# Kernel optimization log

Measured on AMD Instinct MI355X. Metric: run time of the kernel, lower is better.

The kernel has to match this reference:

```python
import jax, jax.numpy as jnp
import numpy as np


def setup_inputs() -> dict:
    key = jax.random.key(0)
    kq, kk, kv = jax.random.split(key, 3)
    B, H, S, d = 2, 16, 2048, 64
    return {
        "query": jax.random.normal(kq, (B, H, S, d), dtype=jnp.float32),
        "keys": jax.random.normal(kk, (B, H, S, d), dtype=jnp.float32),
        "vals": jax.random.normal(kv, (B, H, S, d), dtype=jnp.float32),
    }


def reference(query, keys, vals):
    # SE (RBF-like) kernel attention, include_magnitude=True, p=2, dropout=0 (eval).
    d = query.shape[-1]
    scale = 2.0 * (d ** 0.5)
    q2 = jnp.sum(query * query, axis=-1)  # [B,H,Sq] = ||q||^2
    k2 = jnp.sum(keys * keys, axis=-1)    # [B,H,Sk] = ||k||^2
    qk = jnp.einsum("bhqd,bhkd->bhqk", query, keys)  # [B,H,Sq,Sk]
    # ||q-k||^2 = ||q||^2 - 2 q.k + ||k||^2 ; clamp for numerical safety
    sq_dist = jnp.maximum(q2[..., :, None] - 2.0 * qk + k2[..., None, :], 0.0)
    dist = jnp.sqrt(sq_dist)  # L2 norm (NOT squared), as in torch.norm(diff, p=2)
    # preattn = -||q-k|| / (2 sqrt(d)) + (||q||^2 + ||k||^2) / (2 sqrt(d))
    preattn = (-dist + q2[..., :, None] + k2[..., None, :]) / scale
    attn = jax.nn.softmax(preattn, axis=-1)  # [B,H,Sq,Sk]
    return jnp.einsum("bhqk,bhkd->bhqd", attn, vals)
```

## Files before the change

kernel.cpp:

```cpp
#include <hip/hip_runtime.h>
#include <hip/hip_bf16.h>
#include <math.h>


typedef __attribute__((ext_vector_type(8))) short bf16x8;
typedef __attribute__((ext_vector_type(4))) float f32x4;
typedef __attribute__((ext_vector_type(16))) float f32x16;
typedef __attribute__((ext_vector_type(4))) unsigned int uint32x4;
typedef __attribute__((ext_vector_type(2))) unsigned int uint32x2;

#define SEQ    2048
#define DIM    64
#define NHEAD  32
#define QBLK   128
#define KVB    64
#define NKT    (SEQ / KVB)
#define TILE_B 8192
#define C2     0.0901684403f

__device__ __forceinline__ float fast_exp2(float x) { return __builtin_amdgcn_exp2f(x); }
__device__ __forceinline__ float fast_sqrt(float x) { return __builtin_amdgcn_sqrtf(x); }

__device__ __forceinline__ unsigned int f2bf(float f) {
    __hip_bfloat16 h = __float2bfloat16(f);
    unsigned short u;
    __builtin_memcpy(&u, &h, 2);
    return (unsigned int)u;
}

__device__ __forceinline__ bf16x8 pack4(unsigned a, unsigned b, unsigned c, unsigned d) {
    uint32x4 t; t[0] = a; t[1] = b; t[2] = c; t[3] = d;
    bf16x8 r;
    __builtin_memcpy(&r, &t, 16);
    return r;
}

__global__ __launch_bounds__(256, 4)
void prep_kv(const float* __restrict__ Kg, const float* __restrict__ Vg,
             char* __restrict__ Kp, char* __restrict__ Vp,
             float* __restrict__ k2g) {
    const int tid  = threadIdx.x;
    const int kt   = blockIdx.x;
    const int head = blockIdx.y;
    const size_t hb = (size_t)head * (SEQ * DIM);
    char* kdst = Kp + (size_t)(head * NKT + kt) * TILE_B;
    char* vdst = Vp + (size_t)(head * NKT + kt) * TILE_B;

    {
        const int row = tid >> 2;
        const int sc4 = tid & 3;
        const float* kp = Kg + hb + (size_t)(kt * KVB + row) * DIM + sc4 * 16;
        f32x4 a = *(const f32x4*)kp;
        f32x4 b = *(const f32x4*)(kp + 4);
        f32x4 c = *(const f32x4*)(kp + 8);
        f32x4 d = *(const f32x4*)(kp + 12);
        float part = 0.f;
#pragma unroll
        for (int j = 0; j < 4; ++j)
            part += a[j]*a[j] + b[j]*b[j] + c[j]*c[j] + d[j]*d[j];
        part += __shfl_xor(part, 1);
        part += __shfl_xor(part, 2);
        if (sc4 == 0) k2g[head * SEQ + kt * KVB + row] = part;

        bf16x8 p0, p1;
#pragma unroll
        for (int j = 0; j < 4; ++j) {
            p0[j]     = (short)f2bf(a[j]);
            p0[4 + j] = (short)f2bf(b[j]);
            p1[j]     = (short)f2bf(c[j]);
            p1[4 + j] = (short)f2bf(d[j]);
        }
        const int t = row >> 5;
        char* base = kdst + (t * 4 + sc4) * 1024 + (row & 31) * 16;
        *(bf16x8*)base         = p0;
        *(bf16x8*)(base + 512) = p1;
    }
    {
        const int kp_ = tid & 31;
        const int dg  = tid >> 5;
        const float* vp = Vg + hb + (size_t)(kt * KVB + 2 * kp_) * DIM + dg * 8;
        f32x4 a0 = *(const f32x4*)vp;
        f32x4 a1 = *(const f32x4*)(vp + 4);
        f32x4 b0 = *(const f32x4*)(vp + DIM);
        f32x4 b1 = *(const f32x4*)(vp + DIM + 4);
        const int ks   = kp_ >> 3;
        const int lh   = (kp_ >> 2) & 1;
        const int j    = kp_ & 3;
#pragma unroll
        for (int e = 0; e < 8; ++e) {
            const float lo = (e < 4) ? a0[e] : a1[e - 4];
            const float hi = (e < 4) ? b0[e] : b1[e - 4];
            const unsigned pk = f2bf(lo) | (f2bf(hi) << 16);
            const int d    = dg * 8 + e;
            const int half = d >> 5;
            const int l    = (d & 31) + 32 * lh;
            *(unsigned*)(vdst + (ks * 2 + half) * 1024 + l * 16 + j * 4) = pk;
        }
    }
}

__global__ __launch_bounds__(256, 2)
void se_attn_main(const float* __restrict__ Qg, const char* __restrict__ Kp,
                  const char* __restrict__ Vp, const float* __restrict__ k2g,
                  float* __restrict__ Og) {
    __shared__ float linv_sh[4][32];

    const int tid = threadIdx.x;
    const int w   = tid >> 6;
    const int l   = tid & 63;
    const int ql  = l & 31;
    const int hi  = l >> 5;

    const int bid  = blockIdx.x;
    const int wg   = (bid & 7) * 64 + (bid >> 3);
    const int head = wg >> 4;
    const int qb   = wg & 15;

    const size_t hb = (size_t)head * (SEQ * DIM);
    const int qbase = qb * QBLK + w * 32;

    const char*  Kph = Kp + (size_t)head * NKT * TILE_B;
    const char*  Vph = Vp + (size_t)head * NKT * TILE_B;
    const float* k2h = k2g + head * SEQ;

    bf16x8 qf[4];
    float q2 = 0.f;
#pragma unroll
    for (int s = 0; s < 4; ++s) {
        const float* qp = Qg + hb + (size_t)(qbase + ql) * DIM + s * 16 + hi * 8;
        f32x4 a = *(const f32x4*)qp;
        f32x4 b = *(const f32x4*)(qp + 4);
#pragma unroll
        for (int j = 0; j < 4; ++j) {
            q2 += a[j] * a[j] + b[j] * b[j];
            qf[s][j]     = (short)f2bf(a[j]);
            qf[s][4 + j] = (short)f2bf(b[j]);
        }
    }
    q2 += __shfl_xor(q2, 32);

    f32x16 o0, o1;
#pragma unroll
    for (int i = 0; i < 16; ++i) { o0[i] = 0.f; o1[i] = 0.f; }
    float lsA = 0.f, lsB = 0.f;

    const int loff = l * 16;

    for (int kt = 0; kt < NKT; ++kt) {
        const char* Kt = Kph + (size_t)kt * TILE_B;
        const char* Vt = Vph + (size_t)kt * TILE_B;

        f32x4 k2q[2][4];
#pragma unroll
        for (int t = 0; t < 2; ++t)
#pragma unroll
            for (int rq = 0; rq < 4; ++rq)
                k2q[t][rq] = *(const f32x4*)(k2h + kt * 64 + t * 32 + rq * 8 + 4 * hi);

        f32x16 st0, st1;
#pragma unroll
        for (int i = 0; i < 16; ++i) { st0[i] = 0.f; st1[i] = 0.f; }
        __builtin_amdgcn_s_setprio(1);
#pragma unroll
        for (int s = 0; s < 4; ++s) {
            bf16x8 kf0 = *(const bf16x8*)(Kt + (0 * 4 + s) * 1024 + loff);
            st0 = __builtin_amdgcn_mfma_f32_32x32x16_bf16(kf0, qf[s], st0, 0, 0, 0);
            bf16x8 kf1 = *(const bf16x8*)(Kt + (1 * 4 + s) * 1024 + loff);
            st1 = __builtin_amdgcn_mfma_f32_32x32x16_bf16(kf1, qf[s], st1, 0, 0, 0);
        }
        __builtin_amdgcn_s_setprio(0);

        bf16x8 vf0[4], vf1[4];
#pragma unroll
        for (int ks = 0; ks < 4; ++ks) {
            vf0[ks] = *(const bf16x8*)(Vt + (ks * 2 + 0) * 1024 + loff);
            vf1[ks] = *(const bf16x8*)(Vt + (ks * 2 + 1) * 1024 + loff);
        }

        unsigned cpk[2][4][2];
#pragma unroll
        for (int t = 0; t < 2; ++t) {
#pragma unroll
            for (int rq = 0; rq < 4; ++rq) {
                float pv[4];
#pragma unroll
                for (int r = 0; r < 4; ++r) {
                    const float dot = (t == 0) ? st0[rq * 4 + r] : st1[rq * 4 + r];
                    const float kk  = k2q[t][rq][r];
                    const float sq  = fmaxf(fmaf(-2.f, dot, q2 + kk), 0.f);
                    const float p   = fast_exp2(fmaf(-C2, fast_sqrt(sq), kk * C2));
                    if (r & 1) lsB += p; else lsA += p;
                    pv[r] = p;
                }
                cpk[t][rq][0] = f2bf(pv[0]) | (f2bf(pv[1]) << 16);
                cpk[t][rq][1] = f2bf(pv[2]) | (f2bf(pv[3]) << 16);
            }
        }

        bf16x8 pa[4];
#pragma unroll
        for (int t = 0; t < 2; ++t) {
#pragma unroll
            for (int e = 0; e < 2; ++e) {
                unsigned lo_[2][2], hi_[2][2];
#pragma unroll
                for (int po = 0; po < 2; ++po) {
#pragma unroll
                    for (int i = 0; i < 2; ++i) {
                        uint32x2 r2 = __builtin_amdgcn_permlane32_swap(
                            cpk[t][2 * e + po][i], cpk[t][2 * e + po][i], false, false);
                        lo_[po][i] = r2[0];
                        hi_[po][i] = r2[1];
                    }
                }
                const int ks = t * 2 + e;
                const unsigned u0 = hi ? lo_[1][0] : lo_[0][0];
                const unsigned u1 = hi ? lo_[1][1] : lo_[0][1];
                const unsigned u2 = hi ? hi_[1][0] : hi_[0][0];
                const unsigned u3 = hi ? hi_[1][1] : hi_[0][1];
                pa[ks] = pack4(u0, u1, u2, u3);
            }
        }

        __builtin_amdgcn_s_setprio(1);
#pragma unroll
        for (int ks = 0; ks < 4; ++ks) {
            o0 = __builtin_amdgcn_mfma_f32_32x32x16_bf16(pa[ks], vf0[ks], o0, 0, 0, 0);
            o1 = __builtin_amdgcn_mfma_f32_32x32x16_bf16(pa[ks], vf1[ks], o1, 0, 0, 0);
        }
        __builtin_amdgcn_s_setprio(0);
    }

    float ls = lsA + lsB;
    ls += __shfl_xor(ls, 32);
    const float inv = 1.f / ls;
    if (hi == 0) linv_sh[w][ql] = inv;
    f32x4 iq[4];
#pragma unroll
    for (int rq = 0; rq < 4; ++rq)
        iq[rq] = *(const f32x4*)(&linv_sh[w][rq * 8 + 4 * hi]);

#pragma unroll
    for (int reg = 0; reg < 16; ++reg) {
        const int qloc = (reg & 3) + 8 * (reg >> 2) + 4 * hi;
        float* orow = Og + hb + (size_t)(qbase + qloc) * DIM;
        const float s = iq[reg >> 2][reg & 3];
        orow[ql]      = o0[reg] * s;
        orow[32 + ql] = o1[reg] * s;
    }
}

__global__ __launch_bounds__(256, 4)
void se_attn_mfma(const float* __restrict__ Qg, const float* __restrict__ Kg,
                  const float* __restrict__ Vg, float* __restrict__ Og) {
    __shared__ char  Kl[KVB * 128];
    __shared__ char  Vt[DIM * 128];
    __shared__ char  Pl[4][16 * 128];
    __shared__ float k2s[KVB];

    const int tid = threadIdx.x;
    const int w   = tid >> 6;
    const int l   = tid & 63;
    const int lq  = l & 15;
    const int g   = l >> 4;
    const size_t hb = (size_t)blockIdx.y * (SEQ * DIM);
    const int q = blockIdx.x * 64 + w * 16 + lq;
    char* Pw = Pl[w];
    const int swq = (lq & 7) << 4;

    bf16x8 qf[2];
    float q2 = 0.f;
#pragma unroll
    for (int h = 0; h < 2; ++h) {
        const float* qp = Qg + hb + (size_t)q * DIM + h * 32 + g * 8;
        f32x4 a = *(const f32x4*)qp;
        f32x4 b = *(const f32x4*)(qp + 4);
#pragma unroll
        for (int j = 0; j < 4; ++j) {
            q2 += a[j] * a[j] + b[j] * b[j];
            qf[h][j]     = (short)f2bf(a[j]);
            qf[h][4 + j] = (short)f2bf(b[j]);
        }
    }
    q2 += __shfl_xor(q2, 16);
    q2 += __shfl_xor(q2, 32);

    f32x4 ofr[4];
#pragma unroll
    for (int i = 0; i < 4; ++i) ofr[i] = (f32x4){0.f, 0.f, 0.f, 0.f};
    float m = -INFINITY, lsum = 0.f;

    const int srow = tid >> 2;
    const int sc4  = tid & 3;
    const int vpr  = tid & 31;
    const int vd0  = (tid >> 5) * 8;

    for (int kt = 0; kt < NKT; ++kt) {
        __syncthreads();
        {
            const float* kp = Kg + hb + (size_t)(kt * KVB + srow) * DIM + sc4 * 16;
            f32x4 a = *(const f32x4*)kp;
            f32x4 b = *(const f32x4*)(kp + 4);
            f32x4 c = *(const f32x4*)(kp + 8);
            f32x4 d = *(const f32x4*)(kp + 12);
            float part = 0.f;
#pragma unroll
            for (int j = 0; j < 4; ++j)
                part += a[j]*a[j] + b[j]*b[j] + c[j]*c[j] + d[j]*d[j];
            part += __shfl_xor(part, 1);
            part += __shfl_xor(part, 2);
            if (sc4 == 0) k2s[srow] = part;
            bf16x8 p0, p1;
#pragma unroll
            for (int j = 0; j < 4; ++j) {
                p0[j]     = (short)f2bf(a[j]);
                p0[4 + j] = (short)f2bf(b[j]);
                p1[j]     = (short)f2bf(c[j]);
                p1[4 + j] = (short)f2bf(d[j]);
            }
            const int sw = (srow & 7) << 4;
            const int wa = srow * 128 + sc4 * 32;
            *(bf16x8*)(Kl + (wa ^ sw))        = p0;
            *(bf16x8*)(Kl + ((wa + 16) ^ sw)) = p1;
        }
        {
            const float* vp = Vg + hb + (size_t)(kt * KVB + 2 * vpr) * DIM + vd0;
            f32x4 a0 = *(const f32x4*)vp;
            f32x4 a1 = *(const f32x4*)(vp + 4);
            f32x4 b0 = *(const f32x4*)(vp + DIM);
            f32x4 b1 = *(const f32x4*)(vp + DIM + 4);
#pragma unroll
            for (int j = 0; j < 8; ++j) {
                const float lo = (j < 4) ? a0[j] : a1[j - 4];
                const float hi2 = (j < 4) ? b0[j] : b1[j - 4];
                const unsigned int pk = f2bf(lo) | (f2bf(hi2) << 16);
                const int d = vd0 + j;
                const int wa = d * 128 + vpr * 4;
                *(unsigned int*)(Vt + (wa ^ ((d & 7) << 4))) = pk;
            }
        }
        __syncthreads();

        f32x4 st[4];
#pragma unroll
        for (int f = 0; f < 4; ++f) st[f] = (f32x4){0.f, 0.f, 0.f, 0.f};
#pragma unroll
        for (int f = 0; f < 4; ++f) {
#pragma unroll
            for (int h = 0; h < 2; ++h) {
                const int ra = (f * 16 + lq) * 128 + h * 64 + g * 16;
                bf16x8 kf = *(const bf16x8*)(Kl + (ra ^ swq));
                st[f] = __builtin_amdgcn_mfma_f32_16x16x32_bf16(kf, qf[h], st[f], 0, 0, 0);
            }
        }

        float sc[4][4];
        float tmax = -INFINITY;
#pragma unroll
        for (int f = 0; f < 4; ++f) {
            const f32x4 k2v = *(const f32x4*)(k2s + f * 16 + g * 4);
#pragma unroll
            for (int r = 0; r < 4; ++r) {
                const float kk = k2v[r];
                const float sq = fmaxf(fmaf(-2.f, st[f][r], q2 + kk), 0.f);
                const float s  = (kk - sqrtf(sq)) * 0.0625f;
                sc[f][r] = s;
                tmax = fmaxf(tmax, s);
            }
        }
        tmax = fmaxf(tmax, __shfl_xor(tmax, 16));
        tmax = fmaxf(tmax, __shfl_xor(tmax, 32));
        const float nm    = fmaxf(m, tmax);
        const float scale = __expf(m - nm);
        m = nm;
        lsum *= scale;
#pragma unroll
        for (int i = 0; i < 4; ++i) {
            ofr[i][0] *= scale; ofr[i][1] *= scale;
            ofr[i][2] *= scale; ofr[i][3] *= scale;
        }
#pragma unroll
        for (int f = 0; f < 4; ++f) {
#pragma unroll
            for (int e = 0; e < 2; ++e) {
                const float p0 = __expf(sc[f][2 * e]     - m);
                const float p1 = __expf(sc[f][2 * e + 1] - m);
                lsum += p0 + p1;
                const unsigned int pk = f2bf(p0) | (f2bf(p1) << 16);
                const int pr = 8 * f + 2 * g + e;
                const int wa = lq * 128 + pr * 4;
                *(unsigned int*)(Pw + (wa ^ swq)) = pk;
            }
        }

        bf16x8 pf[2];
#pragma unroll
        for (int h = 0; h < 2; ++h) {
            const int ra = lq * 128 + h * 64 + g * 16;
            pf[h] = *(const bf16x8*)(Pw + (ra ^ swq));
        }
#pragma unroll
        for (int db = 0; db < 4; ++db) {
#pragma unroll
            for (int h = 0; h < 2; ++h) {
                const int ra = (db * 16 + lq) * 128 + h * 64 + g * 16;
                bf16x8 vf = *(const bf16x8*)(Vt + (ra ^ swq));
                ofr[db] = __builtin_amdgcn_mfma_f32_16x16x32_bf16(vf, pf[h], ofr[db], 0, 0, 0);
            }
        }
    }

    lsum += __shfl_xor(lsum, 16);
    lsum += __shfl_xor(lsum, 32);
    const float inv = 1.f / lsum;
    float* op = Og + hb + (size_t)q * DIM;
#pragma unroll
    for (int db = 0; db < 4; ++db) {
#pragma unroll
        for (int r = 0; r < 4; ++r) {
            op[db * 16 + g * 4 + r] = ofr[db][r] * inv;
        }
    }
}

extern "C" void kernel_launch(void* const* d_in, const int* in_sizes, int n_in,
                              void* d_out, int out_size, void* d_ws, size_t ws_size,
                              hipStream_t stream) {
    const float* Q = (const float*)d_in[0];
    const float* K = (const float*)d_in[1];
    const float* V = (const float*)d_in[2];
    float* O = (float*)d_out;

    const size_t KP_B = (size_t)NHEAD * NKT * TILE_B;
    const size_t K2_B = (size_t)NHEAD * SEQ * 4;
    const size_t need = 2 * KP_B + K2_B;

    if (ws_size >= need) {
        char*  Kp = (char*)d_ws;
        char*  Vp = Kp + KP_B;
        float* k2 = (float*)(Kp + 2 * KP_B);
        prep_kv<<<dim3(NKT, NHEAD), 256, 0, stream>>>(K, V, Kp, Vp, k2);
        se_attn_main<<<dim3((SEQ / QBLK) * NHEAD), 256, 0, stream>>>(Q, Kp, Vp, k2, O);
    } else {
        se_attn_mfma<<<dim3(SEQ / 64, NHEAD), 256, 0, stream>>>(Q, K, V, O);
    }
}
```

Baseline: 85.80 us.

## Split KV range across two wave groups per block and reduce via LDS

Doubles the block to 512 threads. Each group of four waves handles half of the KV tiles for the same 32-row query slabs, and the two partial outputs and row sums are combined through swizzled shared memory before normalization. Because the softmax has no running max, partial sums add directly. This doubles the number of waves in flight so memory latency and the exp/sqrt work are hidden better. The cost is an extra 32KB of LDS per block, a barrier, and an LDS reduction pass at the end, and occupancy may be limited by LDS or registers.

```diff
diff --git a/kernel.cpp b/kernel.cpp
--- a/kernel.cpp
+++ b/kernel.cpp
@@ -99,14 +99,18 @@
     }
 }
 
-__global__ __launch_bounds__(256, 2)
+__global__ __launch_bounds__(512, 4)
 void se_attn_main(const float* __restrict__ Qg, const char* __restrict__ Kp,
                   const char* __restrict__ Vp, const float* __restrict__ k2g,
                   float* __restrict__ Og) {
+    __shared__ char  Osh[4][8192];
+    __shared__ float lsp[4][32];
     __shared__ float linv_sh[4][32];
 
     const int tid = threadIdx.x;
     const int w   = tid >> 6;
+    const int qg  = w & 3;
+    const int kh  = w >> 2;
     const int l   = tid & 63;
     const int ql  = l & 31;
     const int hi  = l >> 5;
@@ -117,7 +121,7 @@
     const int qb   = wg & 15;
 
     const size_t hb = (size_t)head * (SEQ * DIM);
-    const int qbase = qb * QBLK + w * 32;
+    const int qbase = qb * QBLK + qg * 32;
 
     const char*  Kph = Kp + (size_t)head * NKT * TILE_B;
     const char*  Vph = Vp + (size_t)head * NKT * TILE_B;
@@ -146,7 +150,8 @@
 
     const int loff = l * 16;
 
-    for (int kt = 0; kt < NKT; ++kt) {
+    for (int i = 0; i < NKT / 2; ++i) {
+        const int kt = kh * (NKT / 2) + i;
         const char* Kt = Kph + (size_t)kt * TILE_B;
         const char* Vt = Vph + (size_t)kt * TILE_B;
 
@@ -159,7 +164,7 @@
 
         f32x16 st0, st1;
 #pragma unroll
-        for (int i = 0; i < 16; ++i) { st0[i] = 0.f; st1[i] = 0.f; }
+        for (int j = 0; j < 16; ++j) { st0[j] = 0.f; st1[j] = 0.f; }
         __builtin_amdgcn_s_setprio(1);
 #pragma unroll
         for (int s = 0; s < 4; ++s) {
@@ -206,11 +211,11 @@
 #pragma unroll
                 for (int po = 0; po < 2; ++po) {
 #pragma unroll
-                    for (int i = 0; i < 2; ++i) {
+                    for (int j = 0; j < 2; ++j) {
                         uint32x2 r2 = __builtin_amdgcn_permlane32_swap(
-                            cpk[t][2 * e + po][i], cpk[t][2 * e + po][i], false, false);
-                        lo_[po][i] = r2[0];
-                        hi_[po][i] = r2[1];
+                            cpk[t][2 * e + po][j], cpk[t][2 * e + po][j], false, false);
+                        lo_[po][j] = r2[0];
+                        hi_[po][j] = r2[1];
                     }
                 }
                 const int ks = t * 2 + e;
@@ -233,20 +238,47 @@
 
     float ls = lsA + lsB;
     ls += __shfl_xor(ls, 32);
-    const float inv = 1.f / ls;
-    if (hi == 0) linv_sh[w][ql] = inv;
-    f32x4 iq[4];
-#pragma unroll
-    for (int rq = 0; rq < 4; ++rq)
-        iq[rq] = *(const f32x4*)(&linv_sh[w][rq * 8 + 4 * hi]);
-
-#pragma unroll
-    for (int reg = 0; reg < 16; ++reg) {
-        const int qloc = (reg & 3) + 8 * (reg >> 2) + 4 * hi;
-        float* orow = Og + hb + (size_t)(qbase + qloc) * DIM;
-        const float s = iq[reg >> 2][reg & 3];
-        orow[ql]      = o0[reg] * s;
-        orow[32 + ql] = o1[reg] * s;
+
+    const int swz = (ql & 7) << 4;
+    char* Oq = Osh[qg];
+
+    if (kh == 1) {
+#pragma unroll
+        for (int qd = 0; qd < 4; ++qd) {
+            const int off = ((8 * qd + 4 * hi) * 4) ^ swz;
+            f32x4 v0, v1;
+#pragma unroll
+            for (int r = 0; r < 4; ++r) { v0[r] = o0[4 * qd + r]; v1[r] = o1[4 * qd + r]; }
+            *(f32x4*)(Oq + ql * 128 + off)        = v0;
+            *(f32x4*)(Oq + (32 + ql) * 128 + off) = v1;
+        }
+        if (hi == 0) lsp[qg][ql] = ls;
+    }
+    __syncthreads();
+    if (kh == 0) {
+        ls += lsp[qg][ql];
+        const float inv = 1.f / ls;
+        if (hi == 0) linv_sh[qg][ql] = inv;
+#pragma unroll
+        for (int qd = 0; qd < 4; ++qd) {
+            const int off = ((8 * qd + 4 * hi) * 4) ^ swz;
+            f32x4 v0 = *(const f32x4*)(Oq + ql * 128 + off);
+            f32x4 v1 = *(const f32x4*)(Oq + (32 + ql) * 128 + off);
+#pragma unroll
+            for (int r = 0; r < 4; ++r) { o0[4 * qd + r] += v0[r]; o1[4 * qd + r] += v1[r]; }
+        }
+        f32x4 iq[4];
+#pragma unroll
+        for (int rq = 0; rq < 4; ++rq)
+            iq[rq] = *(const f32x4*)(&linv_sh[qg][rq * 8 + 4 * hi]);
+#pragma unroll
+        for (int reg = 0; reg < 16; ++reg) {
+            const int qloc = (reg & 3) + 8 * (reg >> 2) + 4 * hi;
+            float* orow = Og + hb + (size_t)(qbase + qloc) * DIM;
+            const float s = iq[reg >> 2][reg & 3];
+            orow[ql]      = o0[reg] * s;
+            orow[32 + ql] = o1[reg] * s;
+        }
     }
 }
 
@@ -440,7 +472,7 @@
         char*  Vp = Kp + KP_B;
         float* k2 = (float*)(Kp + 2 * KP_B);
         prep_kv<<<dim3(NKT, NHEAD), 256, 0, stream>>>(K, V, Kp, Vp, k2);
-        se_attn_main<<<dim3((SEQ / QBLK) * NHEAD), 256, 0, stream>>>(Q, Kp, Vp, k2, O);
+        se_attn_main<<<dim3((SEQ / QBLK) * NHEAD), 512, 0, stream>>>(Q, Kp, Vp, k2, O);
     } else {
         se_attn_mfma<<<dim3(SEQ / 64, NHEAD), 256, 0, stream>>>(Q, K, V, O);
     }
```

Result: slower. 227.4 us (+165.0%).
